# Optimization experiments

Measured on AMD Instinct MI355X. Metric: run time of the kernel, lower is better.

Reference implementation:

```python
import jax, jax.numpy as jnp
import numpy as np

NUM_HEADS = 8
D_MODEL = 256
D_K = 256
SEQ = 32
FFT_HEAD = 3  # heads >= 3 operate in the FFT domain and are IFFT'd after
NEG = jnp.float32(1e10)


def _fft_t(x):
    # x: (..., 32, 256) real. Interleaved real/imag pairs -> complex 2D FFT over (4,2).
    lead = x.shape[:-2]
    xr = x.reshape(lead + (16, 32, 4, 2, 2))
    xc = jax.lax.complex(xr[..., 0], xr[..., 1])      # (..., 16, 32, 4, 2)
    y = jnp.fft.fft2(xc)                              # over last two axes
    out = jnp.concatenate([jnp.real(y), jnp.imag(y)], axis=-1)  # (...,16,32,4,4)
    return out.reshape(lead + (SEQ, D_MODEL))


def _ifft_t(x):
    lead = x.shape[:-2]
    xr = x.reshape(lead + (16, 32, 4, 2, 2))
    xc = jax.lax.complex(xr[..., 0], xr[..., 1])
    y = jnp.fft.ifft2(xc)
    out = jnp.concatenate([jnp.real(y), jnp.imag(y)], axis=-1)
    return out.reshape(lead + (SEQ, D_MODEL))


def _atrous_mask():
    i = jnp.arange(SEQ)[:, None]
    j = jnp.arange(SEQ)[None, :]
    return (jnp.abs(i - j) % 2 == 0).astype(jnp.float32)  # (32, 32)


def _attn_group(x, Wq_g, Wk_g, Wv_g, mask):
    # x: (B, S, D); W*_g: (H, D, K); mask: (S, S)
    Q = jnp.einsum('bsd,hdk->bhsk', x, Wq_g)
    K = jnp.einsum('bsd,hdk->bhsk', x, Wk_g)
    V = jnp.einsum('bsd,hdk->bhsk', x, Wv_g)
    scores = jnp.einsum('bhsk,bhtk->bhst', Q, K) / jnp.sqrt(jnp.float32(D_K))
    scores = scores * mask - NEG * (1.0 - mask)
    A = jax.nn.softmax(scores, axis=-1)
    return jnp.einsum('bhst,bhtk->bhsk', A, V)  # (B, H, S, K)


def setup_inputs() -> dict:
    key = jax.random.key(0)
    k0, k1, k2, k3 = jax.random.split(key, 4)
    B = 4096
    glorot = float(np.sqrt(2.0 / (D_MODEL + D_K)))
    return {
        'inputs': jax.random.normal(k0, (B, 1, SEQ, D_MODEL), dtype=jnp.float32),
        'Wq': jax.random.normal(k1, (NUM_HEADS, D_MODEL, D_K), dtype=jnp.float32) * glorot,
        'Wk': jax.random.normal(k2, (NUM_HEADS, D_MODEL, D_K), dtype=jnp.float32) * glorot,
        'Wv': jax.random.normal(k3, (NUM_HEADS, D_MODEL, D_K), dtype=jnp.float32) * glorot,
    }


def reference(inputs, Wq, Wk, Wv):
    # inputs: (B, 1, 32, 256)
    x = inputs[:, 0]                                  # (B, 32, 256)
    mask = _atrous_mask()
    # Heads 0..2: plain domain
    out_lo = _attn_group(x, Wq[:FFT_HEAD], Wk[:FFT_HEAD], Wv[:FFT_HEAD], mask)
    # Heads 3..: FFT domain, outputs IFFT'd per head
    xf = _fft_t(x)
    out_hi = _attn_group(xf, Wq[FFT_HEAD:], Wk[FFT_HEAD:], Wv[FFT_HEAD:], mask)
    out_hi = _ifft_t(out_hi)
    total = out_lo.sum(axis=1) + out_hi.sum(axis=1)   # (B, 32, 256)
    return (total / NUM_HEADS)[:, None]               # (B, 1, 32, 256)
```

## Files before the change

### kernel.cpp

```cpp
#include <hip/hip_runtime.h>

typedef _Float16 f16;
typedef _Float16 f16x4 __attribute__((ext_vector_type(4)));
typedef _Float16 f16x8 __attribute__((ext_vector_type(8)));
typedef float    f32x4 __attribute__((ext_vector_type(4)));
typedef unsigned int u32;

#define MFMA_F16(a,b,c) __builtin_amdgcn_mfma_f32_16x16x32_f16((a),(b),(c),0,0,0)

__device__ __forceinline__ u32 pkf16(float a, float b) {
  return __builtin_bit_cast(u32, __builtin_amdgcn_cvt_pkrtz(a, b));
}
union F8U4 { u32 d[4]; f16x8 v; };

__device__ __forceinline__ f16x8 comb(f16x4 a, f16x4 b) {
  f16x8 r;
  #pragma unroll
  for (int i = 0; i < 4; ++i) { r[i] = a[i]; r[4 + i] = b[i]; }
  return r;
}

__device__ __forceinline__ float T_val(int rr, int cc) {
  int p = rr >> 2, f = rr & 3;
  int c = cc >> 2, d = (cc >> 1) & 1, e = cc & 1;
  int q = f & 1;
  int m = (p * c + 2 * q * d) & 3;
  float cs = (m == 0) ? 1.f : (m == 2) ? -1.f : 0.f;
  float sn = (m == 1) ? 1.f : (m == 3) ? -1.f : 0.f;
  if (f < 2) return (e == 0) ? cs : sn;
  return (e == 0) ? -sn : cs;
}
__device__ __forceinline__ float U_val(int rr, int cc) {
  int p = rr >> 2, f = rr & 3;
  int c = cc >> 2, d = (cc >> 1) & 1, e = cc & 1;
  int q = f & 1;
  int m = (p * c + 2 * q * d) & 3;
  float cs = (m == 0) ? 1.f : (m == 2) ? -1.f : 0.f;
  float sn = (m == 1) ? 1.f : (m == 3) ? -1.f : 0.f;
  float v;
  if (f < 2) v = (e == 0) ? cs : -sn;
  else       v = (e == 0) ? sn : cs;
  return v * 0.125f;
}

__global__ void prep_qk(const float* __restrict__ Wq, const float* __restrict__ Wk,
                        float* __restrict__ WqE, float* __restrict__ WkE) {
  int b = blockIdx.x;
  int isK = b >> 11;
  int h = (b >> 8) & 7;
  int dd = b & 255;
  const float* W = isK ? Wk : Wq;
  float* E = isK ? WkE : WqE;
  int k = threadIdx.x;
  size_t base = (size_t)h * 65536;
  float v;
  if (h < 3) {
    v = W[base + (size_t)dd * 256 + k];
  } else {
    int g = dd >> 4, i = dd & 15;
    float s = 0.f;
    for (int ip = 0; ip < 16; ++ip) {
      float t = T_val(ip, i);
      if (t != 0.f) s += t * W[base + (size_t)(g * 16 + ip) * 256 + k];
    }
    v = s;
  }
  E[base + (size_t)dd * 256 + k] = v;
}

__global__ void prep_m(const float* __restrict__ WqE, const float* __restrict__ WkE,
                       f16* __restrict__ Mt) {
  __shared__ float Aq[32][33];
  __shared__ float Bk[32][33];
  int h = blockIdx.x >> 6;
  int dpt = (blockIdx.x >> 3) & 7;
  int dt = blockIdx.x & 7;
  int tid = threadIdx.x;
  int drow = tid & 31;
  int dprow4 = (tid >> 5) * 4;
  float acc0 = 0.f, acc1 = 0.f, acc2 = 0.f, acc3 = 0.f;
  int r = tid >> 3;
  int c0 = (tid & 7) * 4;
  for (int kt = 0; kt < 8; ++kt) {
    for (int jj = 0; jj < 4; ++jj) {
      Aq[r][c0 + jj] = WqE[(size_t)h * 65536 + (size_t)(dt * 32 + r) * 256 + kt * 32 + c0 + jj];
      Bk[r][c0 + jj] = WkE[(size_t)h * 65536 + (size_t)(dpt * 32 + r) * 256 + kt * 32 + c0 + jj];
    }
    __syncthreads();
    #pragma unroll
    for (int k = 0; k < 32; ++k) {
      float a = Aq[drow][k];
      acc0 += a * Bk[dprow4 + 0][k];
      acc1 += a * Bk[dprow4 + 1][k];
      acc2 += a * Bk[dprow4 + 2][k];
      acc3 += a * Bk[dprow4 + 3][k];
    }
    __syncthreads();
  }
  int d_ = dt * 32 + drow;
  size_t ob = (size_t)h * 65536 + (size_t)(dpt * 32 + dprow4) * 256 + d_;
  Mt[ob + 0 * 256] = (f16)(acc0 * 0.0625f);
  Mt[ob + 1 * 256] = (f16)(acc1 * 0.0625f);
  Mt[ob + 2 * 256] = (f16)(acc2 * 0.0625f);
  Mt[ob + 3 * 256] = (f16)(acc3 * 0.0625f);
}

__global__ void prep_v(const float* __restrict__ Wv, f16* __restrict__ Wvt) {
  __shared__ float Ts[16][16];
  __shared__ float Us[16][16];
  int h = blockIdx.x >> 8;
  int kp = blockIdx.x & 255;
  int tid = threadIdx.x;
  Ts[tid >> 4][tid & 15] = T_val(tid >> 4, tid & 15);
  Us[tid >> 4][tid & 15] = U_val(tid >> 4, tid & 15);
  __syncthreads();
  int d = tid;
  int g = d >> 4, i = d & 15;
  int gp = kp >> 4, fp = kp & 15;
  float s = 0.f;
  if (h < 3) {
    s = Wv[(size_t)h * 65536 + (size_t)d * 256 + kp];
  } else {
    for (int ip = 0; ip < 16; ++ip) {
      float tv = Ts[ip][i];
      if (tv != 0.f) {
        float inner = 0.f;
        for (int jj = 0; jj < 16; ++jj) {
          float uv = Us[fp][jj];
          if (uv != 0.f)
            inner += uv * Wv[(size_t)h * 65536 + (size_t)(g * 16 + ip) * 256 + gp * 16 + jj];
        }
        s += tv * inner;
      }
    }
  }
  Wvt[(size_t)h * 65536 + (size_t)kp * 256 + d] = (f16)(s * 0.125f);
}

__global__ void repack16(const f16* __restrict__ Mt, const f16* __restrict__ Wvt,
                         f16* __restrict__ MtF, f16* __restrict__ WvF) {
  int bid = blockIdx.x;
  int which = bid >> 10;
  int h = (bid >> 7) & 7;
  int t16 = (bid >> 3) & 15;
  int kt = bid & 7;
  int l = threadIdx.x;
  const f16* src = which ? Wvt : Mt;
  f16* dst = which ? WvF : MtF;
  size_t sb = (size_t)h * 65536 + (size_t)(t16 * 16 + (l & 15)) * 256 + kt * 32 + (l >> 4) * 8;
  size_t db = ((size_t)((h * 16 + t16) * 8 + kt) * 64 + l) * 8;
  *(f16x8*)(dst + db) = *(const f16x8*)(src + sb);
}

__global__ __launch_bounds__(512, 4) void mha_main(
    const float* __restrict__ xg_all,
    const f16* __restrict__ MtF,
    const f16* __restrict__ WvF,
    float* __restrict__ outG)
{
  extern __shared__ char smem[];
  f16* Xs  = (f16*)smem;
  f16* Y   = (f16*)(smem + 32768);
  f16* Aat = (f16*)(smem + 65536);

  const int tid = threadIdx.x;
  const int w   = tid >> 6;
  const int l   = tid & 63;
  const int l15 = l & 15;
  const int l4  = l >> 4;

  const float* xg = xg_all + (size_t)blockIdx.x * 16384;
  #pragma unroll 4
  for (int i = 0; i < 8; ++i) {
    int f4 = i * 512 + tid;
    int row = f4 >> 6;
    int col = (f4 & 63) << 2;
    f32x4 v = *(const f32x4*)(xg + (size_t)f4 * 4);
    f16x4 hv;
    hv[0] = (f16)v[0]; hv[1] = (f16)v[1]; hv[2] = (f16)v[2]; hv[3] = (f16)v[3];
    *(f16x4*)(Xs + row * 256 + (col ^ ((row & 7) << 3))) = hv;
  }
  __syncthreads();

  const int bq = w >> 2, mt = (w >> 1) & 1, rh = w & 1;

  f32x4 O[2][2][2];
  #pragma unroll
  for (int b = 0; b < 2; ++b)
    #pragma unroll
    for (int sm = 0; sm < 2; ++sm)
      #pragma unroll
      for (int n = 0; n < 2; ++n)
        O[b][sm][n] = (f32x4){0.f, 0.f, 0.f, 0.f};

  for (int h = 0; h < 8; ++h) {
    {
      f32x4 C[2][4];
      #pragma unroll
      for (int a = 0; a < 2; ++a)
        #pragma unroll
        for (int n = 0; n < 4; ++n) C[a][n] = (f32x4){0.f, 0.f, 0.f, 0.f};
      #pragma unroll 2
      for (int kt = 0; kt < 8; ++kt) {
        f16x8 A[2], B[4];
        #pragma unroll
        for (int a = 0; a < 2; ++a)
          A[a] = *(const f16x8*)(MtF + ((size_t)((h * 16 + w * 2 + a) * 8 + kt) * 64 + l) * 8);
        #pragma unroll
        for (int n = 0; n < 4; ++n) {
          int srow = n * 16 + l15;
          B[n] = *(const f16x8*)(Xs + srow * 256 + ((kt * 32 + l4 * 8) ^ ((srow & 7) << 3)));
        }
        __builtin_amdgcn_s_setprio(1);
        #pragma unroll
        for (int a = 0; a < 2; ++a)
          #pragma unroll
          for (int n = 0; n < 4; ++n)
            C[a][n] = MFMA_F16(A[a], B[n], C[a][n]);
        __builtin_amdgcn_s_setprio(0);
      }
      #pragma unroll
      for (int a = 0; a < 2; ++a)
        #pragma unroll
        for (int n = 0; n < 4; ++n) {
          int srow = n * 16 + l15;
          int dcol = (w * 2 + a) * 16 + l4 * 4;
          f16x4 hv;
          hv[0] = (f16)C[a][n][0]; hv[1] = (f16)C[a][n][1];
          hv[2] = (f16)C[a][n][2]; hv[3] = (f16)C[a][n][3];
          *(f16x4*)(Y + srow * 256 + (dcol ^ ((srow & 7) << 3))) = hv;
        }
    }
    u32 Vh[4][2][2];
    {
      f32x4 VC[4][2];
      #pragma unroll
      for (int tau = 0; tau < 4; ++tau)
        #pragma unroll
        for (int n = 0; n < 2; ++n) VC[tau][n] = (f32x4){0.f, 0.f, 0.f, 0.f};
      #pragma unroll 2
      for (int kt = 0; kt < 8; ++kt) {
        f16x8 Bw[2], Ax[4];
        #pragma unroll
        for (int n = 0; n < 2; ++n)
          Bw[n] = *(const f16x8*)(WvF + ((size_t)((h * 16 + w * 2 + n) * 8 + kt) * 64 + l) * 8);
        #pragma unroll
        for (int tau = 0; tau < 4; ++tau) {
          int xrow = tau * 16 + l15;
          Ax[tau] = *(const f16x8*)(Xs + xrow * 256 + ((kt * 32 + l4 * 8) ^ ((xrow & 7) << 3)));
        }
        __builtin_amdgcn_s_setprio(1);
        #pragma unroll
        for (int tau = 0; tau < 4; ++tau)
          #pragma unroll
          for (int n = 0; n < 2; ++n)
            VC[tau][n] = MFMA_F16(Ax[tau], Bw[n], VC[tau][n]);
        __builtin_amdgcn_s_setprio(0);
      }
      #pragma unroll
      for (int tau = 0; tau < 4; ++tau)
        #pragma unroll
        for (int n = 0; n < 2; ++n) {
          Vh[tau][n][0] = pkf16(VC[tau][n][0], VC[tau][n][1]);
          Vh[tau][n][1] = pkf16(VC[tau][n][2], VC[tau][n][3]);
        }
    }
    __syncthreads();

    {
      f32x4 S0 = (f32x4){0.f, 0.f, 0.f, 0.f};
      f32x4 S1 = (f32x4){0.f, 0.f, 0.f, 0.f};
      int yrow = bq * 32 + mt * 16 + l15;
      int x0 = bq * 32 + l15;
      int x1 = bq * 32 + 16 + l15;
      #pragma unroll
      for (int kt = 0; kt < 8; ++kt) {
        int ks = kt * 32 + l4 * 8;
        f16x8 ay = *(const f16x8*)(Y + yrow * 256 + (ks ^ ((yrow & 7) << 3)));
        f16x8 b0 = *(const f16x8*)(Xs + x0 * 256 + (ks ^ ((x0 & 7) << 3)));
        f16x8 b1 = *(const f16x8*)(Xs + x1 * 256 + (ks ^ ((x1 & 7) << 3)));
        S0 = MFMA_F16(ay, b0, S0);
        S1 = MFMA_F16(ay, b1, S1);
      }
      #pragma unroll
      for (int rr = 0; rr < 2; ++rr) {
        int r = rh * 2 + rr;
        bool valid = ((l & 1) == (r & 1));
        float v0 = valid ? S0[r] : -1e30f;
        float v1 = valid ? S1[r] : -1e30f;
        float mx = fmaxf(v0, v1);
        mx = fmaxf(mx, __shfl_xor(mx, 1));
        mx = fmaxf(mx, __shfl_xor(mx, 2));
        mx = fmaxf(mx, __shfl_xor(mx, 4));
        mx = fmaxf(mx, __shfl_xor(mx, 8));
        float e0 = valid ? __expf(v0 - mx) : 0.f;
        float e1 = valid ? __expf(v1 - mx) : 0.f;
        float sm = e0 + e1;
        sm += __shfl_xor(sm, 1);
        sm += __shfl_xor(sm, 2);
        sm += __shfl_xor(sm, 4);
        sm += __shfl_xor(sm, 8);
        float inv = 1.f / sm;
        int s = mt * 16 + l4 * 4 + r;
        Aat[(bq * 32 + s) * 40 + l15] = (f16)(e0 * inv);
        Aat[(bq * 32 + s) * 40 + 16 + l15] = (f16)(e1 * inv);
      }
    }
    __syncthreads();

    #pragma unroll
    for (int b = 0; b < 2; ++b) {
      #pragma unroll
      for (int sm = 0; sm < 2; ++sm) {
        int arow = (b * 32 + sm * 16 + l15) * 40 + l4 * 4;
        f16x8 bf = comb(*(const f16x4*)(Aat + arow),
                        *(const f16x4*)(Aat + arow + 16));
        #pragma unroll
        for (int n = 0; n < 2; ++n) {
          F8U4 av;
          av.d[0] = Vh[b * 2 + 0][n][0];
          av.d[1] = Vh[b * 2 + 0][n][1];
          av.d[2] = Vh[b * 2 + 1][n][0];
          av.d[3] = Vh[b * 2 + 1][n][1];
          O[b][sm][n] = MFMA_F16(av.v, bf, O[b][sm][n]);
        }
      }
    }
  }

  #pragma unroll
  for (int b = 0; b < 2; ++b) {
    float* ob = outG + ((size_t)blockIdx.x * 2 + b) * 8192;
    #pragma unroll
    for (int sm = 0; sm < 2; ++sm) {
      int s = sm * 16 + l15;
      #pragma unroll
      for (int n = 0; n < 2; ++n) {
        int kp = w * 32 + n * 16 + l4 * 4;
        *(f32x4*)(ob + s * 256 + kp) = O[b][sm][n];
      }
    }
  }
}

extern "C" void kernel_launch(void* const* d_in, const int* in_sizes, int n_in,
                              void* d_out, int out_size, void* d_ws, size_t ws_size,
                              hipStream_t stream) {
  const float* x  = (const float*)d_in[0];
  const float* Wq = (const float*)d_in[1];
  const float* Wk = (const float*)d_in[2];
  const float* Wv = (const float*)d_in[3];
  float* out = (float*)d_out;
  char* ws = (char*)d_ws;
  float* WqE = (float*)ws;
  float* WkE = (float*)(ws + 2097152);
  f16*   Mt  = (f16*)(ws + 4194304);
  f16*   Wvt = (f16*)(ws + 5242880);
  f16*   MtF = (f16*)ws;
  f16*   WvF = (f16*)(ws + 2097152);

  prep_qk<<<4096, 256, 0, stream>>>(Wq, Wk, WqE, WkE);
  prep_m<<<512, 256, 0, stream>>>(WqE, WkE, Mt);
  prep_v<<<2048, 256, 0, stream>>>(Wv, Wvt);
  repack16<<<2048, 64, 0, stream>>>(Mt, Wvt, MtF, WvF);
  mha_main<<<2048, 512, 70656, stream>>>(x, MtF, WvF, out);
}
```

Baseline: 406.2 us.

## Use 32x32x16 MFMA for Y=M·X projection and concentrate softmax in four waves

Switches the per-head Y projection from 16x16x32 MFMAs to 32x32x16 MFMAs, with a new repack kernel producing a matching 32-row weight fragment layout. Each wave now loads one A fragment per k-step and reuses it across two 32-row B tiles, which halves the global weight fragment traffic. The score/softmax phase now runs on only four waves, each handling all four accumulator rows, and the Aat row pitch shrinks from 40 to 36 halves, reducing LDS. The risks are idle waves during softmax and possible bank conflicts from the new pitch.

```diff
diff --git a/kernel.cpp b/kernel.cpp
--- a/kernel.cpp
+++ b/kernel.cpp
@@ -4,9 +4,11 @@
 typedef _Float16 f16x4 __attribute__((ext_vector_type(4)));
 typedef _Float16 f16x8 __attribute__((ext_vector_type(8)));
 typedef float    f32x4 __attribute__((ext_vector_type(4)));
+typedef float    f32x16 __attribute__((ext_vector_type(16)));
 typedef unsigned int u32;
 
-#define MFMA_F16(a,b,c) __builtin_amdgcn_mfma_f32_16x16x32_f16((a),(b),(c),0,0,0)
+#define MFMA_F16(a,b,c)  __builtin_amdgcn_mfma_f32_16x16x32_f16((a),(b),(c),0,0,0)
+#define MFMA32(a,b,c)    __builtin_amdgcn_mfma_f32_32x32x16_f16((a),(b),(c),0,0,0)
 
 __device__ __forceinline__ u32 pkf16(float a, float b) {
   return __builtin_bit_cast(u32, __builtin_amdgcn_cvt_pkrtz(a, b));
@@ -137,24 +139,31 @@
   Wvt[(size_t)h * 65536 + (size_t)kp * 256 + d] = (f16)(s * 0.125f);
 }
 
-__global__ void repack16(const f16* __restrict__ Mt, const f16* __restrict__ Wvt,
-                         f16* __restrict__ MtF, f16* __restrict__ WvF) {
+__global__ void repackV(const f16* __restrict__ Wvt, f16* __restrict__ WvF) {
   int bid = blockIdx.x;
-  int which = bid >> 10;
   int h = (bid >> 7) & 7;
   int t16 = (bid >> 3) & 15;
   int kt = bid & 7;
   int l = threadIdx.x;
-  const f16* src = which ? Wvt : Mt;
-  f16* dst = which ? WvF : MtF;
   size_t sb = (size_t)h * 65536 + (size_t)(t16 * 16 + (l & 15)) * 256 + kt * 32 + (l >> 4) * 8;
   size_t db = ((size_t)((h * 16 + t16) * 8 + kt) * 64 + l) * 8;
-  *(f16x8*)(dst + db) = *(const f16x8*)(src + sb);
+  *(f16x8*)(WvF + db) = *(const f16x8*)(Wvt + sb);
+}
+
+__global__ void repackM32(const f16* __restrict__ Mt, f16* __restrict__ MtF32) {
+  int bid = blockIdx.x;
+  int h = (bid >> 7) & 7;
+  int dpt = (bid >> 4) & 7;
+  int kt = bid & 15;
+  int l = threadIdx.x;
+  size_t sb = (size_t)h * 65536 + (size_t)(dpt * 32 + (l & 31)) * 256 + kt * 16 + (l >> 5) * 8;
+  size_t db = ((size_t)((h * 8 + dpt) * 16 + kt) * 64 + l) * 8;
+  *(f16x8*)(MtF32 + db) = *(const f16x8*)(Mt + sb);
 }
 
 __global__ __launch_bounds__(512, 4) void mha_main(
     const float* __restrict__ xg_all,
-    const f16* __restrict__ MtF,
+    const f16* __restrict__ MtF32,
     const f16* __restrict__ WvF,
     float* __restrict__ outG)
 {
@@ -168,6 +177,8 @@
   const int l   = tid & 63;
   const int l15 = l & 15;
   const int l4  = l >> 4;
+  const int l31 = l & 31;
+  const int hi  = l >> 5;
 
   const float* xg = xg_all + (size_t)blockIdx.x * 16384;
   #pragma unroll 4
@@ -182,7 +193,7 @@
   }
   __syncthreads();
 
-  const int bq = w >> 2, mt = (w >> 1) & 1, rh = w & 1;
+  const int bq = w >> 1, mt = w & 1;
 
   f32x4 O[2][2][2];
   #pragma unroll
@@ -195,41 +206,32 @@
 
   for (int h = 0; h < 8; ++h) {
     {
-      f32x4 C[2][4];
-      #pragma unroll
-      for (int a = 0; a < 2; ++a)
-        #pragma unroll
-        for (int n = 0; n < 4; ++n) C[a][n] = (f32x4){0.f, 0.f, 0.f, 0.f};
-      #pragma unroll 2
-      for (int kt = 0; kt < 8; ++kt) {
-        f16x8 A[2], B[4];
-        #pragma unroll
-        for (int a = 0; a < 2; ++a)
-          A[a] = *(const f16x8*)(MtF + ((size_t)((h * 16 + w * 2 + a) * 8 + kt) * 64 + l) * 8);
-        #pragma unroll
-        for (int n = 0; n < 4; ++n) {
-          int srow = n * 16 + l15;
-          B[n] = *(const f16x8*)(Xs + srow * 256 + ((kt * 32 + l4 * 8) ^ ((srow & 7) << 3)));
-        }
+      f32x16 C0, C1;
+      #pragma unroll
+      for (int i = 0; i < 16; ++i) { C0[i] = 0.f; C1[i] = 0.f; }
+      const f16* Abase = MtF32 + ((size_t)((h * 8 + w) * 16) * 64 + l) * 8;
+      #pragma unroll 4
+      for (int kt = 0; kt < 16; ++kt) {
+        f16x8 A = *(const f16x8*)(Abase + kt * 512);
+        int cb = kt * 16 + hi * 8;
+        f16x8 B0 = *(const f16x8*)(Xs + l31 * 256 + (cb ^ ((l31 & 7) << 3)));
+        int r1 = 32 + l31;
+        f16x8 B1 = *(const f16x8*)(Xs + r1 * 256 + (cb ^ ((r1 & 7) << 3)));
         __builtin_amdgcn_s_setprio(1);
-        #pragma unroll
-        for (int a = 0; a < 2; ++a)
-          #pragma unroll
-          for (int n = 0; n < 4; ++n)
-            C[a][n] = MFMA_F16(A[a], B[n], C[a][n]);
+        C0 = MFMA32(A, B0, C0);
+        C1 = MFMA32(A, B1, C1);
         __builtin_amdgcn_s_setprio(0);
       }
       #pragma unroll
-      for (int a = 0; a < 2; ++a)
-        #pragma unroll
-        for (int n = 0; n < 4; ++n) {
-          int srow = n * 16 + l15;
-          int dcol = (w * 2 + a) * 16 + l4 * 4;
-          f16x4 hv;
-          hv[0] = (f16)C[a][n][0]; hv[1] = (f16)C[a][n][1];
-          hv[2] = (f16)C[a][n][2]; hv[3] = (f16)C[a][n][3];
-          *(f16x4*)(Y + srow * 256 + (dcol ^ ((srow & 7) << 3))) = hv;
-        }
+      for (int q = 0; q < 4; ++q) {
+        int dcol = w * 32 + q * 8 + hi * 4;
+        f16x4 h0, h1;
+        #pragma unroll
+        for (int j = 0; j < 4; ++j) { h0[j] = (f16)C0[q * 4 + j]; h1[j] = (f16)C1[q * 4 + j]; }
+        int s0 = l31, s1 = 32 + l31;
+        *(f16x4*)(Y + s0 * 256 + (dcol ^ ((s0 & 7) << 3))) = h0;
+        *(f16x4*)(Y + s1 * 256 + (dcol ^ ((s1 & 7) << 3))) = h1;
+      }
     }
     u32 Vh[4][2][2];
     {
@@ -267,7 +269,7 @@
     }
     __syncthreads();
 
-    {
+    if (w < 4) {
       f32x4 S0 = (f32x4){0.f, 0.f, 0.f, 0.f};
       f32x4 S1 = (f32x4){0.f, 0.f, 0.f, 0.f};
       int yrow = bq * 32 + mt * 16 + l15;
@@ -283,8 +285,7 @@
         S1 = MFMA_F16(ay, b1, S1);
       }
       #pragma unroll
-      for (int rr = 0; rr < 2; ++rr) {
-        int r = rh * 2 + rr;
+      for (int r = 0; r < 4; ++r) {
         bool valid = ((l & 1) == (r & 1));
         float v0 = valid ? S0[r] : -1e30f;
         float v1 = valid ? S1[r] : -1e30f;
@@ -302,8 +303,8 @@
         sm += __shfl_xor(sm, 8);
         float inv = 1.f / sm;
         int s = mt * 16 + l4 * 4 + r;
-        Aat[(bq * 32 + s) * 40 + l15] = (f16)(e0 * inv);
-        Aat[(bq * 32 + s) * 40 + 16 + l15] = (f16)(e1 * inv);
+        Aat[(bq * 32 + s) * 36 + l15] = (f16)(e0 * inv);
+        Aat[(bq * 32 + s) * 36 + 16 + l15] = (f16)(e1 * inv);
       }
     }
     __syncthreads();
@@ -312,7 +313,7 @@
     for (int b = 0; b < 2; ++b) {
       #pragma unroll
       for (int sm = 0; sm < 2; ++sm) {
-        int arow = (b * 32 + sm * 16 + l15) * 40 + l4 * 4;
+        int arow = (b * 32 + sm * 16 + l15) * 36 + l4 * 4;
         f16x8 bf = comb(*(const f16x4*)(Aat + arow),
                         *(const f16x4*)(Aat + arow + 16));
         #pragma unroll
@@ -356,12 +357,13 @@
   float* WkE = (float*)(ws + 2097152);
   f16*   Mt  = (f16*)(ws + 4194304);
   f16*   Wvt = (f16*)(ws + 5242880);
-  f16*   MtF = (f16*)ws;
-  f16*   WvF = (f16*)(ws + 2097152);
+  f16*   MtF32 = (f16*)ws;
+  f16*   WvF   = (f16*)(ws + 2097152);
 
   prep_qk<<<4096, 256, 0, stream>>>(Wq, Wk, WqE, WkE);
   prep_m<<<512, 256, 0, stream>>>(WqE, WkE, Mt);
   prep_v<<<2048, 256, 0, stream>>>(Wv, Wvt);
-  repack16<<<2048, 64, 0, stream>>>(Mt, Wvt, MtF, WvF);
-  mha_main<<<2048, 512, 70656, stream>>>(x, MtF, WvF, out);
-}
+  repackM32<<<1024, 64, 0, stream>>>(Mt, MtF32);
+  repackV<<<1024, 64, 0, stream>>>(Wvt, WvF);
+  mha_main<<<2048, 512, 70144, stream>>>(x, MtF32, WvF, out);
+}
```

Result: slower. 441.9 us (+8.8%).
